# Optimization experiments

Hardware: AMD Instinct MI355X
Metric: run time of the kernel (lower is better)

Reference implementation:

```python
import jax, jax.numpy as jnp
import numpy as np

# cfg constants reconstructed from the repo's YOLOv2 (VOC) setup
ANCHORS = jnp.array([[1.3221, 1.73145], [3.19275, 4.00944], [5.05587, 8.09892],
                     [9.47112, 4.84053], [11.2364, 10.0071]], dtype=jnp.float32)
NUM_CLASSES = 20
LAMBDA_COORD = 5.0
LAMBDA_OBJ = 1.0
LAMBDA_NOOBJ = 0.5
LAMBDA_CLS = 1.0

B, H, W = 256, 26, 26
A = 5


def setup_inputs() -> dict:
    key = jax.random.key(0)
    k1, k2, k3, k4, k5 = jax.random.split(key, 5)
    prediction = jax.random.normal(k1, (B, A * (5 + NUM_CLASSES), H, W), dtype=jnp.float32)
    # build a realistic target: [...,:20] one-hot class, [...,20] conf in {0,1}, [...,21:23] xy in (0,1), [...,23:25] wh>0
    conf = (jax.random.uniform(k2, (B, H, W, 1)) < 0.03).astype(jnp.float32)
    xy = jax.random.uniform(k3, (B, H, W, 2), dtype=jnp.float32)
    wh = jax.random.uniform(k4, (B, H, W, 2), dtype=jnp.float32) * 6.0 + 0.5
    labels = jax.random.randint(k5, (B, H, W), 0, NUM_CLASSES)
    cls = jax.nn.one_hot(labels, NUM_CLASSES, dtype=jnp.float32)
    target = jnp.concatenate([cls, conf, xy, wh], axis=-1)  # [B,H,W,25]
    return {"prediction": prediction, "target": target}


def _box_iou(a, b):
    # a: [B,H,W,A,4] (cx,cy,w,h), b: [B,H,W,1,4] -> iou [B,H,W,A]
    ax1, ay1 = a[..., 0] - a[..., 2] / 2, a[..., 1] - a[..., 3] / 2
    ax2, ay2 = a[..., 0] + a[..., 2] / 2, a[..., 1] + a[..., 3] / 2
    bx1, by1 = b[..., 0] - b[..., 2] / 2, b[..., 1] - b[..., 3] / 2
    bx2, by2 = b[..., 0] + b[..., 2] / 2, b[..., 1] + b[..., 3] / 2
    iw = jnp.clip(jnp.minimum(ax2, bx2) - jnp.maximum(ax1, bx1), 0.0)
    ih = jnp.clip(jnp.minimum(ay2, by2) - jnp.maximum(ay1, by1), 0.0)
    inter = iw * ih
    union = a[..., 2] * a[..., 3] + b[..., 2] * b[..., 3] - inter
    return inter / (union + 1e-10)


def reference(prediction, target):
    bsize = prediction.shape[0]
    out = prediction.transpose(0, 2, 3, 1).reshape(bsize, H, W, A, 5 + NUM_CLASSES)
    pred_conf = jax.nn.sigmoid(out[..., 20])                      # [B,H,W,A]
    pred_xy = jax.nn.sigmoid(out[..., 21:23])                     # [B,H,W,A,2]
    pred_wh = jnp.exp(out[..., 23:25]) * ANCHORS                  # generate_anchorbox: wh scaled by anchor priors
    pred_cls = out[..., :20]                                      # [B,H,W,A,20]
    pred_box = jnp.concatenate([pred_xy, pred_wh], axis=-1)       # [B,H,W,A,4]

    tgt = target[:, :, :, None, :]                                # unsqueeze_(3)
    gt_conf = tgt[..., 20]                                        # [B,H,W,1]
    gt_box = jnp.concatenate([tgt[..., 21:23], tgt[..., 23:25]], axis=-1)  # [B,H,W,1,4]
    gt_cls = tgt[..., :20]                                        # [B,H,W,1,20]

    obj = (gt_conf[..., 0] != 0).astype(prediction.dtype)         # [B,H,W] (nonzero mask)

    iou = _box_iou(pred_box, gt_box)                              # [B,H,W,A]
    aidx = jnp.argmax(iou, axis=-1)                               # [B,H,W]

    best_box = jnp.take_along_axis(pred_box, aidx[..., None, None], axis=3)[:, :, :, 0]   # [B,H,W,4]
    best_conf = jnp.take_along_axis(pred_conf, aidx[..., None], axis=3)[:, :, :, 0]       # [B,H,W]
    best_cls = jnp.take_along_axis(pred_cls, aidx[..., None, None], axis=3)[:, :, :, 0]   # [B,H,W,20]

    box_loss = LAMBDA_COORD / bsize * jnp.sum(obj[..., None] * (best_box - gt_box[:, :, :, 0]) ** 2)
    conf_loss = LAMBDA_OBJ / bsize * jnp.sum(obj * (best_conf - gt_conf[..., 0]) ** 2)
    noobj_loss = LAMBDA_NOOBJ / bsize * jnp.sum((1.0 - obj) * best_conf ** 2)

    labels = jnp.argmax(gt_cls[:, :, :, 0], axis=-1)              # [B,H,W]
    logp = jax.nn.log_softmax(best_cls, axis=-1)
    nll = -jnp.take_along_axis(logp, labels[..., None], axis=-1)[..., 0]
    cls_loss = LAMBDA_CLS / bsize * jnp.sum(obj * nll)

    return (box_loss, conf_loss, noobj_loss, cls_loss)
```

## Files before the change

kernel.cpp:

```cpp
#include <hip/hip_runtime.h>
#include <math.h>

#define NHW 676
#define NB 256
#define NCELLS (NB * NHW)
#define NC 20
#define NA 5

__device__ __forceinline__ float sigmoidf_(float x) {
    return 1.0f / (1.0f + __expf(-x));
}

__global__ __launch_bounds__(256) void yolo_loss_kernel(
    const float* __restrict__ pred,
    const float* __restrict__ tgt,
    float* __restrict__ out)
{
    const float AW[NA] = {1.3221f, 3.19275f, 5.05587f, 9.47112f, 11.2364f};
    const float AH[NA] = {1.73145f, 4.00944f, 8.09892f, 4.84053f, 10.0071f};

    const int t = blockIdx.x * blockDim.x + threadIdx.x;
    const int b  = t / NHW;
    const int hw = t - b * NHW;
    const float* p  = pred + (size_t)b * 125 * NHW + hw;
    const float* tg = tgt + (size_t)t * 25;

    float v[NA][5];
    #pragma unroll
    for (int a = 0; a < NA; ++a) {
        #pragma unroll
        for (int c = 0; c < 5; ++c) {
            v[a][c] = p[(a * 25 + 20 + c) * NHW];
        }
    }
    float gconf = tg[20];
    float gx = tg[21], gy = tg[22], gw = tg[23], gh = tg[24];

    float g_x1 = gx - gw * 0.5f, g_x2 = gx + gw * 0.5f;
    float g_y1 = gy - gh * 0.5f, g_y2 = gy + gh * 0.5f;
    float g_area = gw * gh;

    float best_iou = -1.0f;
    int   best_a = 0;
    float bx = 0, by = 0, bw = 0, bh = 0, btc = 0;

    #pragma unroll
    for (int a = 0; a < NA; ++a) {
        float px = sigmoidf_(v[a][1]);
        float py = sigmoidf_(v[a][2]);
        float pw = __expf(v[a][3]) * AW[a];
        float ph = __expf(v[a][4]) * AH[a];
        float iw = fminf(px + pw * 0.5f, g_x2) - fmaxf(px - pw * 0.5f, g_x1);
        float ih = fminf(py + ph * 0.5f, g_y2) - fmaxf(py - ph * 0.5f, g_y1);
        iw = fmaxf(iw, 0.0f);
        ih = fmaxf(ih, 0.0f);
        float inter = iw * ih;
        float uni = pw * ph + g_area - inter;
        float iou = inter / (uni + 1e-10f);
        if (iou > best_iou) {
            best_iou = iou;
            best_a = a;
            bx = px; by = py; bw = pw; bh = ph;
            btc = v[a][0];
        }
    }
    float bconf = sigmoidf_(btc);

    float box_l = 0.0f, conf_l = 0.0f, noobj_l = 0.0f, cls_l = 0.0f;

    if (gconf != 0.0f) {
        float dx = bx - gx, dy = by - gy, dw = bw - gw, dh = bh - gh;
        box_l = dx * dx + dy * dy + dw * dw + dh * dh;
        float dc = bconf - gconf;
        conf_l = dc * dc;

        const float* pc = p + best_a * 25 * NHW;
        float lg[NC], oh[NC];
        #pragma unroll
        for (int k = 0; k < NC; ++k) lg[k] = pc[k * NHW];
        #pragma unroll
        for (int k = 0; k < NC; ++k) oh[k] = tg[k];

        float m = lg[0];
        #pragma unroll
        for (int k = 1; k < NC; ++k) m = fmaxf(m, lg[k]);
        float s = 0.0f, l_sel = 0.0f;
        #pragma unroll
        for (int k = 0; k < NC; ++k) {
            s += __expf(lg[k] - m);
            if (oh[k] > 0.5f) l_sel = lg[k];
        }
        cls_l = -(l_sel - m - __logf(s));
    } else {
        noobj_l = bconf * bconf;
    }

    #pragma unroll
    for (int off = 32; off > 0; off >>= 1) {
        box_l   += __shfl_down(box_l,   off, 64);
        conf_l  += __shfl_down(conf_l,  off, 64);
        noobj_l += __shfl_down(noobj_l, off, 64);
        cls_l   += __shfl_down(cls_l,   off, 64);
    }

    __shared__ float sred[4][4];
    int wave = threadIdx.x >> 6;
    int lane = threadIdx.x & 63;
    if (lane == 0) {
        sred[wave][0] = box_l;
        sred[wave][1] = conf_l;
        sred[wave][2] = noobj_l;
        sred[wave][3] = cls_l;
    }
    __syncthreads();
    if (threadIdx.x == 0) {
        float b0 = 0, b1 = 0, b2 = 0, b3 = 0;
        #pragma unroll
        for (int w = 0; w < 4; ++w) {
            b0 += sred[w][0];
            b1 += sred[w][1];
            b2 += sred[w][2];
            b3 += sred[w][3];
        }
        atomicAdd(&out[0], b0 * (5.0f / 256.0f));
        atomicAdd(&out[1], b1 * (1.0f / 256.0f));
        atomicAdd(&out[2], b2 * (0.5f / 256.0f));
        atomicAdd(&out[3], b3 * (1.0f / 256.0f));
    }
}

extern "C" void kernel_launch(void* const* d_in, const int* in_sizes, int n_in,
                              void* d_out, int out_size, void* d_ws, size_t ws_size,
                              hipStream_t stream) {
    const float* pred = (const float*)d_in[0];
    const float* tgt  = (const float*)d_in[1];
    float* out = (float*)d_out;

    hipMemsetAsync(out, 0, out_size * sizeof(float), stream);

    dim3 grid(NCELLS / 256);
    dim3 block(256);
    hipLaunchKernelGGL(yolo_loss_kernel, grid, block, 0, stream,
                       pred, tgt, out);
}
```

Measured before the change: 156.9 us.

## Stage targets in LDS and prefetch all anchor class logits speculatively

Target rows for the block are copied into shared memory with coalesced float4 loads instead of strided per-thread reads. For object cells, class logits of all five anchors are loaded up front, removing the dependent load after anchor selection, and the softmax NLL is computed for every anchor then selected. A launch-bounds occupancy hint is added. This raises memory traffic and register pressure for waves containing object cells.

Result: no change. 159.4 us (+1.6%).

```diff
diff --git a/kernel.cpp b/kernel.cpp
--- a/kernel.cpp
+++ b/kernel.cpp
@@ -11,7 +11,7 @@
     return 1.0f / (1.0f + __expf(-x));
 }
 
-__global__ __launch_bounds__(256) void yolo_loss_kernel(
+__global__ __launch_bounds__(256, 3) void yolo_loss_kernel(
     const float* __restrict__ pred,
     const float* __restrict__ tgt,
     float* __restrict__ out)
@@ -19,11 +19,15 @@
     const float AW[NA] = {1.3221f, 3.19275f, 5.05587f, 9.47112f, 11.2364f};
     const float AH[NA] = {1.73145f, 4.00944f, 8.09892f, 4.84053f, 10.0071f};
 
-    const int t = blockIdx.x * blockDim.x + threadIdx.x;
-    const int b  = t / NHW;
-    const int hw = t - b * NHW;
-    const float* p  = pred + (size_t)b * 125 * NHW + hw;
-    const float* tg = tgt + (size_t)t * 25;
+    __shared__ __align__(16) float stgt[256 * 25];
+    __shared__ float sred[4][4];
+
+    const int tid = threadIdx.x;
+    const int t0  = blockIdx.x << 8;
+    const int t   = t0 + tid;
+    const int b   = t / NHW;
+    const int hw  = t - b * NHW;
+    const float* p = pred + (size_t)b * 125 * NHW + hw;
 
     float v[NA][5];
     #pragma unroll
@@ -33,12 +37,36 @@
             v[a][c] = p[(a * 25 + 20 + c) * NHW];
         }
     }
-    float gconf = tg[20];
-    float gx = tg[21], gy = tg[22], gw = tg[23], gh = tg[24];
+    const float gconf = tgt[(size_t)t * 25 + 20];
 
-    float g_x1 = gx - gw * 0.5f, g_x2 = gx + gw * 0.5f;
-    float g_y1 = gy - gh * 0.5f, g_y2 = gy + gh * 0.5f;
-    float g_area = gw * gh;
+    {
+        const float4* g4 = (const float4*)(tgt + (size_t)t0 * 25);
+        float4* s4 = (float4*)stgt;
+        #pragma unroll
+        for (int i = 0; i < 6; ++i) s4[i * 256 + tid] = g4[i * 256 + tid];
+        if (tid < 64) s4[1536 + tid] = g4[1536 + tid];
+    }
+
+    const bool obj = (gconf != 0.0f);
+
+    float cl[NA][NC];
+    if (obj) {
+        #pragma unroll
+        for (int a = 0; a < NA; ++a) {
+            #pragma unroll
+            for (int k = 0; k < NC; ++k) {
+                cl[a][k] = p[(a * 25 + k) * NHW];
+            }
+        }
+    }
+
+    __syncthreads();
+    const float* tg = stgt + tid * 25;
+
+    const float gx = tg[21], gy = tg[22], gw = tg[23], gh = tg[24];
+    const float g_x1 = gx - gw * 0.5f, g_x2 = gx + gw * 0.5f;
+    const float g_y1 = gy - gh * 0.5f, g_y2 = gy + gh * 0.5f;
+    const float g_area = gw * gh;
 
     float best_iou = -1.0f;
     int   best_a = 0;
@@ -64,33 +92,34 @@
             btc = v[a][0];
         }
     }
-    float bconf = sigmoidf_(btc);
+    const float bconf = sigmoidf_(btc);
 
     float box_l = 0.0f, conf_l = 0.0f, noobj_l = 0.0f, cls_l = 0.0f;
 
-    if (gconf != 0.0f) {
+    if (obj) {
         float dx = bx - gx, dy = by - gy, dw = bw - gw, dh = bh - gh;
         box_l = dx * dx + dy * dy + dw * dw + dh * dh;
         float dc = bconf - gconf;
         conf_l = dc * dc;
 
-        const float* pc = p + best_a * 25 * NHW;
-        float lg[NC], oh[NC];
+        float nll[NA];
         #pragma unroll
-        for (int k = 0; k < NC; ++k) lg[k] = pc[k * NHW];
+        for (int a = 0; a < NA; ++a) {
+            float m = cl[a][0];
+            #pragma unroll
+            for (int k = 1; k < NC; ++k) m = fmaxf(m, cl[a][k]);
+            float s = 0.0f, lsel = 0.0f;
+            #pragma unroll
+            for (int k = 0; k < NC; ++k) {
+                s += __expf(cl[a][k] - m);
+                if (tg[k] > 0.5f) lsel = cl[a][k];
+            }
+            nll[a] = -(lsel - m - __logf(s));
+        }
+        float cls = nll[0];
         #pragma unroll
-        for (int k = 0; k < NC; ++k) oh[k] = tg[k];
-
-        float m = lg[0];
-        #pragma unroll
-        for (int k = 1; k < NC; ++k) m = fmaxf(m, lg[k]);
-        float s = 0.0f, l_sel = 0.0f;
-        #pragma unroll
-        for (int k = 0; k < NC; ++k) {
-            s += __expf(lg[k] - m);
-            if (oh[k] > 0.5f) l_sel = lg[k];
-        }
-        cls_l = -(l_sel - m - __logf(s));
+        for (int a = 1; a < NA; ++a) cls = (best_a == a) ? nll[a] : cls;
+        cls_l = cls;
     } else {
         noobj_l = bconf * bconf;
     }
@@ -103,9 +132,8 @@
         cls_l   += __shfl_down(cls_l,   off, 64);
     }
 
-    __shared__ float sred[4][4];
-    int wave = threadIdx.x >> 6;
-    int lane = threadIdx.x & 63;
+    int wave = tid >> 6;
+    int lane = tid & 63;
     if (lane == 0) {
         sred[wave][0] = box_l;
         sred[wave][1] = conf_l;
@@ -113,7 +141,7 @@
         sred[wave][3] = cls_l;
     }
     __syncthreads();
-    if (threadIdx.x == 0) {
+    if (tid == 0) {
         float b0 = 0, b1 = 0, b2 = 0, b3 = 0;
         #pragma unroll
         for (int w = 0; w < 4; ++w) {
```
